# Performance work log

Hardware: AMD Instinct MI355X
Metric: run time of the kernel (lower is better)

The kernel has to match this reference:

```python
import jax, jax.numpy as jnp
import numpy as np

B, T, V, E, U = 1024, 256, 50000, 512, 1024

def setup_inputs() -> dict:
    key = jax.random.key(0)
    ks = jax.random.split(key, 10)
    s = lambda k, shape, fan: jax.random.normal(k, shape, dtype=jnp.float32) * (1.0 / np.sqrt(fan))
    return {
        "inputs": jax.random.randint(ks[0], (B, T), 0, V, dtype=jnp.int32),
        "emb": s(ks[1], (V, E), E),
        "W0": s(ks[2], (E, U), E),
        "U0": s(ks[3], (U, U), U),
        "b0": jnp.zeros((U,), jnp.float32),
        "W1": s(ks[4], (U, U), U),
        "U1": s(ks[5], (U, U), U),
        "b1": jnp.zeros((U,), jnp.float32),
        "Wout": s(ks[6], (U, 1), U),
        "bout": jnp.zeros((1,), jnp.float32),
    }

def reference(inputs, emb, W0, U0, b0, W1, U1, b1, Wout, bout):
    x = emb[inputs]                      # [B, T, E] embedding lookup
    xT = jnp.swapaxes(x, 0, 1)           # [T, B, E] time-major for scan
    h0_init = jnp.zeros((inputs.shape[0], U0.shape[0]), x.dtype)
    h1_init = jnp.zeros((inputs.shape[0], U1.shape[0]), x.dtype)

    def step(carry, xt):
        h0, h1 = carry
        h0 = jnp.tanh(xt @ W0 + h0 @ U0 + b0)   # SimpleRNNCell 0 (dropout inactive, inference)
        h1 = jnp.tanh(h0 @ W1 + h1 @ U1 + b1)   # SimpleRNNCell 1
        return (h0, h1), None

    (h0, h1), _ = jax.lax.scan(step, (h0_init, h1_init), xT)
    return jax.nn.sigmoid(h1 @ Wout + bout)      # [B, 1]
```

## Files before the change

### kernel.cpp

```cpp
#include <hip/hip_runtime.h>
#include <hip/hip_cooperative_groups.h>
#include <math.h>

namespace cg = cooperative_groups;

typedef unsigned short u16;
typedef __bf16 bf16x8 __attribute__((ext_vector_type(8)));
typedef float f32x4 __attribute__((ext_vector_type(4)));
typedef unsigned short u16x8 __attribute__((ext_vector_type(8)));
typedef int i32x4 __attribute__((ext_vector_type(4)));

#define NBLK 256
#define NTHR 512
#define BB 1024
#define TT 256
#define EE 512
#define UU 1024
#define K0 1536
#define K1 2048
#define NK0 48
#define NK1 64
#define KTL0 32
#define KTL1 16
#define HN0 ((size_t)BB * K0)
#define HN1 ((size_t)BB * K1)
#define LDS_BYTES 163840

#define ROSTER_BASE 0
#define FLAG_BASE 32
#define EPOCH_BASE (32 + 2048)
#define BAR_INTS 2560

#define AUX_SC0 1

__device__ i32x4 llvm_amdgcn_raw_buffer_load_i32x4(i32x4 srsrc, int voffset, int soffset,
                                                   int aux) __asm("llvm.amdgcn.raw.buffer.load.v4i32");

__device__ __forceinline__ i32x4 make_srd(const void* p) {
  union { const void* p; int i[2]; } u; u.p = p;
  i32x4 r; r.x = u.i[0]; r.y = u.i[1]; r.z = -1; r.w = 0x00020000;
  return r;
}

__device__ __forceinline__ u16 f2bf(float f) {
  unsigned u = __builtin_bit_cast(unsigned, f);
  u += 0x7fffu + ((u >> 16) & 1u);
  return (u16)(u >> 16);
}
__device__ __forceinline__ float bf2f(u16 h) {
  return __builtin_bit_cast(float, ((unsigned)h) << 16);
}
__device__ __forceinline__ float fast_tanh(float x) {
  x = fminf(fmaxf(x, -15.f), 15.f);
  float e = __expf(2.f * x);
  return (e - 1.f) / (e + 1.f);
}

template<int K, int KLOW>
__device__ __forceinline__ void wfill(u16* __restrict__ Wt,
    const float* __restrict__ Wl, const float* __restrict__ Wh, int gstart) {
  constexpr int NK = K / 32;
  constexpr int NG = 1024 * K / 8;
  for (int g = gstart; g < NG; g += NBLK * NTHR) {
    const int lane = g & 63;
    const int r = g >> 6;
    const int kt = r % NK;
    const int cb = r / NK;
    const int n = cb * 16 + (lane & 15);
    const int kb = kt * 32 + (lane >> 4) * 8;
    u16x8 o;
#pragma unroll
    for (int e = 0; e < 8; ++e) {
      const int k = kb + e;
      const float v = (k < KLOW) ? Wl[(size_t)k * UU + n] : Wh[(size_t)(k - KLOW) * UU + n];
      o[e] = f2bf(v);
    }
    *(u16x8*)(Wt + (size_t)g * 8) = o;
  }
}

__device__ __forceinline__ void xbar(int* __restrict__ bar, int xcc, int slot, int nx,
                                     int tgt, int tid) {
  __syncthreads();
  if (tid < 64) {
    if (tid == 0)
      __hip_atomic_store(&bar[FLAG_BASE + xcc * 256 + slot], tgt,
                         __ATOMIC_RELAXED, __HIP_MEMORY_SCOPE_AGENT);
    if (slot == 0) {
      for (int base = 0; base < nx; base += 64) {
        const int i = base + tid;
        const bool act = (i < nx);
        int guard = 0;
        bool done = false;
        do {
          int v = act ? __hip_atomic_load(&bar[FLAG_BASE + xcc * 256 + i],
                                          __ATOMIC_RELAXED, __HIP_MEMORY_SCOPE_AGENT)
                      : tgt;
          done = __all(v >= tgt) != 0;
        } while (!done && ++guard < 300000);
      }
      if (tid == 0)
        __hip_atomic_store(&bar[EPOCH_BASE + xcc * 32], tgt,
                           __ATOMIC_RELAXED, __HIP_MEMORY_SCOPE_AGENT);
    } else if (tid == 0) {
      int guard = 0;
      while (__hip_atomic_load(&bar[EPOCH_BASE + xcc * 32],
                               __ATOMIC_RELAXED, __HIP_MEMORY_SCOPE_AGENT) < tgt
             && ++guard < 600000)
        __builtin_amdgcn_s_sleep(8);
    }
  }
  __syncthreads();
}

__device__ __forceinline__ void mf1(const i32x4& av,
    const u16* __restrict__ p0, const u16* __restrict__ p1,
    const u16* __restrict__ q2, const u16* __restrict__ q3,
    size_t koff, int lo, f32x4 (&acc)[4]) {
  u16x8 b0 = *(const u16x8*)(p0 + koff + lo);
  u16x8 b1 = *(const u16x8*)(p1 + koff + lo);
  u16x8 b2 = *(const u16x8*)(q2 + koff + lo);
  u16x8 b3 = *(const u16x8*)(q3 + koff + lo);
  bf16x8 fa0 = __builtin_bit_cast(bf16x8, av);
  bf16x8 fb0 = __builtin_bit_cast(bf16x8, b0);
  bf16x8 fb1 = __builtin_bit_cast(bf16x8, b1);
  bf16x8 fb2 = __builtin_bit_cast(bf16x8, b2);
  bf16x8 fb3 = __builtin_bit_cast(bf16x8, b3);
  acc[0] = __builtin_amdgcn_mfma_f32_16x16x32_bf16(fa0, fb0, acc[0], 0, 0, 0);
  acc[1] = __builtin_amdgcn_mfma_f32_16x16x32_bf16(fa0, fb1, acc[1], 0, 0, 0);
  acc[2] = __builtin_amdgcn_mfma_f32_16x16x32_bf16(fa0, fb2, acc[2], 0, 0, 0);
  acc[3] = __builtin_amdgcn_mfma_f32_16x16x32_bf16(fa0, fb3, acc[3], 0, 0, 0);
}

template<int K, int KTL>
__device__ __forceinline__ void gemm2(const i32x4& srdA, int voA,
    const u16* __restrict__ bA, const u16* __restrict__ bB,
    const u16* __restrict__ bP, int lane, f32x4 (&acc)[4]) {
  constexpr int NK = K / 32;
  constexpr int NG = NK / 8;
  const int lo = lane * 8;
  const u16* p0 = bA;
  const u16* p1 = bA + (size_t)NK * 512;
  const u16* bP3 = bP + (size_t)KTL * 512;
  const u16* bB3 = bB + (size_t)NK * 512;

  i32x4 aE[8], aO[8];
#pragma unroll
  for (int j = 0; j < 8; ++j)
    aE[j] = llvm_amdgcn_raw_buffer_load_i32x4(srdA, voA + j * 64, 0, AUX_SC0);

#pragma unroll
  for (int g = 0; g < NG; ++g) {
    if (g + 1 < NG) {
#pragma unroll
      for (int j = 0; j < 8; ++j) {
        if ((g & 1) == 0)
          aO[j] = llvm_amdgcn_raw_buffer_load_i32x4(srdA, voA + ((g + 1) * 8 + j) * 64, 0, AUX_SC0);
        else
          aE[j] = llvm_amdgcn_raw_buffer_load_i32x4(srdA, voA + ((g + 1) * 8 + j) * 64, 0, AUX_SC0);
      }
    }
#pragma unroll
    for (int j = 0; j < 8; ++j) {
      const int kt = g * 8 + j;
      const bool pre = (KTL > 0) && (kt < KTL);
      const u16* q2 = pre ? bP : bB;
      const u16* q3 = pre ? bP3 : bB3;
      if ((g & 1) == 0) mf1(aE[j], p0, p1, q2, q3, (size_t)kt * 512, lo, acc);
      else              mf1(aO[j], p0, p1, q2, q3, (size_t)kt * 512, lo, acc);
    }
  }
}

__device__ __forceinline__ void do_l0(int tk, int xcc, int jl, bool uselds,
    const u16* __restrict__ ldsb, const u16* __restrict__ Wt0,
    const int* __restrict__ inputs, const float* __restrict__ emb,
    const float* __restrict__ b0, u16* __restrict__ A0, u16* __restrict__ A1,
    int tid)
{
  const int lane = tid & 63, w = tid >> 6, q = lane >> 4, l16 = lane & 15;
  const int c0 = jl * 64;
  if (tk < TT - 1) {
    const int grow = xcc * 128 + jl * 8 + (tid >> 6);
    const int c = (tid & 63) * 8;
    const int idx = inputs[grow * TT + tk + 1];
    const f32x4* s = (const f32x4*)(emb + (size_t)idx * EE + c);
    f32x4 f0 = s[0], f1 = s[1];
    u16x8 oa;
#pragma unroll
    for (int j = 0; j < 4; ++j) { oa[j] = f2bf(f0[j]); oa[j + 4] = f2bf(f1[j]); }
    *(u16x8*)(A0 + (size_t)((tk + 1) & 1) * HN0 + (size_t)grow * K0 + c) = oa;
  }
  if (tk < TT) {
    f32x4 acc[4];
#pragma unroll
    for (int n = 0; n < 4; ++n) acc[n] = (f32x4){0.f, 0.f, 0.f, 0.f};
    i32x4 srdA = make_srd(A0 + (size_t)(tk & 1) * HN0);
    const int voA = ((xcc * 128 + w * 16 + l16) * K0 + q * 8) * 2;
    const u16* gA = Wt0 + (size_t)(c0 / 16) * NK0 * 512;
    const u16* bB = Wt0 + (size_t)(c0 / 16 + 2) * NK0 * 512;
    if (uselds) gemm2<K0, KTL0>(srdA, voA, ldsb, bB,
                                ldsb + (size_t)2 * NK0 * 512, lane, acc);
    else        gemm2<K0, 0   >(srdA, voA, gA, bB, ldsb, lane, acc);
    u16* d1 = A1 + (size_t)(tk & 1) * HN1;
    u16* d2 = A0 + (size_t)((tk + 1) & 1) * HN0 + 512;
#pragma unroll
    for (int n = 0; n < 4; ++n) {
      const int col = c0 + n * 16 + l16;
      const float bs = b0[col];
#pragma unroll
      for (int rr = 0; rr < 4; ++rr) {
        const int grow = xcc * 128 + w * 16 + q * 4 + rr;
        const u16 v = f2bf(fast_tanh(acc[n][rr] + bs));
        d1[(size_t)grow * K1 + col] = v;
        d2[(size_t)grow * K0 + col] = v;
      }
    }
  }
}

__device__ __forceinline__ void do_l1(int tk, int xcc, int jl, bool uselds,
    const u16* __restrict__ ldsb, const u16* __restrict__ Wt1,
    const float* __restrict__ b1, u16* __restrict__ A1, int tid)
{
  const int lane = tid & 63, w = tid >> 6, q = lane >> 4, l16 = lane & 15;
  const int c0 = jl * 64;
  f32x4 acc[4];
#pragma unroll
  for (int n = 0; n < 4; ++n) acc[n] = (f32x4){0.f, 0.f, 0.f, 0.f};
  i32x4 srdA = make_srd(A1 + (size_t)((tk - 1) & 1) * HN1);
  const int voA = ((xcc * 128 + w * 16 + l16) * K1 + q * 8) * 2;
  const u16* gA = Wt1 + (size_t)(c0 / 16) * NK1 * 512;
  const u16* bB = Wt1 + (size_t)(c0 / 16 + 2) * NK1 * 512;
  if (uselds) gemm2<K1, KTL1>(srdA, voA, ldsb, bB,
                              ldsb + (size_t)2 * NK1 * 512, lane, acc);
  else        gemm2<K1, 0   >(srdA, voA, gA, bB, ldsb, lane, acc);
  u16* d1 = A1 + (size_t)(tk & 1) * HN1 + 1024;
#pragma unroll
  for (int n = 0; n < 4; ++n) {
    const int col = c0 + n * 16 + l16;
    const float bs = b1[col];
#pragma unroll
    for (int rr = 0; rr < 4; ++rr) {
      const int grow = xcc * 128 + w * 16 + q * 4 + rr;
      d1[(size_t)grow * K1 + col] = f2bf(fast_tanh(acc[n][rr] + bs));
    }
  }
}

__global__ __launch_bounds__(NTHR, 2)
void rnn_kernel(const int* __restrict__ inputs, const float* __restrict__ emb,
    const float* __restrict__ W0, const float* __restrict__ U0, const float* __restrict__ b0,
    const float* __restrict__ W1, const float* __restrict__ U1, const float* __restrict__ b1,
    const float* __restrict__ Wout, const float* __restrict__ bout,
    float* __restrict__ out,
    u16* __restrict__ Wt0, u16* __restrict__ Wt1,
    u16* __restrict__ A0, u16* __restrict__ A1, int* __restrict__ bar)
{
  extern __shared__ u16 lds[];
  int* li = (int*)lds;
  cg::grid_group grid = cg::this_grid();
  const int tid = threadIdx.x, bid = blockIdx.x;

  const int gstart = bid * NTHR + tid;
  wfill<K0, 512>(Wt0, W0, U0, gstart);
  wfill<K1, 1024>(Wt1, W1, U1, gstart);
  for (int g = gstart; g < BB * EE / 8; g += NBLK * NTHR) {
    const int b = g >> 6, seg = g & 63;
    const int idx = inputs[b * TT];
    const f32x4* s = (const f32x4*)(emb + (size_t)idx * EE + seg * 8);
    f32x4 f0 = s[0], f1 = s[1];
    u16x8 o;
#pragma unroll
    for (int j = 0; j < 4; ++j) { o[j] = f2bf(f0[j]); o[j + 4] = f2bf(f1[j]); }
    *(u16x8*)(A0 + (size_t)b * K0 + seg * 8) = o;
  }
  {
    const u16x8 z = {0, 0, 0, 0, 0, 0, 0, 0};
    for (int g = gstart; g < BB * 1024 / 8; g += NBLK * NTHR) {
      const int b = g >> 7, seg = g & 127;
      *(u16x8*)(A0 + (size_t)b * K0 + 512 + seg * 8) = z;
      *(u16x8*)(A1 + (size_t)b * K1 + 1024 + seg * 8) = z;
    }
  }
  if (bid == 0) for (int i = tid; i < BAR_INTS; i += NTHR) bar[i] = 0;
  grid.sync();

  if (tid == 0) {
    const int xc = __builtin_amdgcn_s_getreg((7 << 11) | 20) & 7;
    li[0] = xc;
    li[1] = atomicAdd(&bar[ROSTER_BASE + xc], 1);
  }
  __syncthreads();
  const int xcc = li[0], slot = li[1];
  __syncthreads();
  grid.sync();
  if (tid == 0)
    li[0] = __hip_atomic_load(&bar[ROSTER_BASE + xcc],
                              __ATOMIC_RELAXED, __HIP_MEMORY_SCOPE_AGENT);
  __syncthreads();
  const int nx = li[0];
  __syncthreads();

  if (slot < 32) {
    const bool pL0 = slot < 16;
    const int cb = (pL0 ? slot : slot - 16) * 4;
    const int NKp = pL0 ? NK0 : NK1;
    const int KTLp = pL0 ? KTL0 : KTL1;
    const u16* W = pL0 ? Wt0 : Wt1;
    const u16x8* s = (const u16x8*)(W + (size_t)cb * NKp * 512);
    const int nv = 2 * NKp * 64;
    u16x8* d = (u16x8*)lds;
    for (int i = tid; i < nv; i += NTHR) d[i] = s[i];
    u16x8* d2 = d + nv;
    const int nv2 = 2 * KTLp * 64;
    for (int i = tid; i < nv2; i += NTHR) {
      const int f = i / (KTLp * 64);
      const int rem = i - f * (KTLp * 64);
      d2[i] = *((const u16x8*)(W + (size_t)(cb + 2 + f) * NKp * 512) + rem);
    }
  }
  __syncthreads();

  for (int tk = 0; tk <= TT; ++tk) {
    for (int job = slot; job < 32; job += nx) {
      const bool uselds = (job == slot);
      if (job < 16) do_l0(tk, xcc, job, uselds, lds, Wt0, inputs, emb, b0, A0, A1, tid);
      else if (tk >= 1) do_l1(tk, xcc, job - 16, uselds, lds, Wt1, b1, A1, tid);
    }
    xbar(bar, xcc, slot, nx, tk + 1, tid);
  }

  if (slot == 0) {
    const int lane = tid & 63, w = tid >> 6;
    i32x4 srdH = make_srd(A1);
    const f32x4* wv = (const f32x4*)(Wout + lane * 16);
    f32x4 w0 = wv[0], w1 = wv[1], w2 = wv[2], w3 = wv[3];
    for (int rr = 0; rr < 16; ++rr) {
      const int grow = xcc * 128 + w * 16 + rr;
      const int vo = (grow * K1 + 1024 + lane * 16) * 2;
      i32x4 hv0 = llvm_amdgcn_raw_buffer_load_i32x4(srdH, vo, 0, AUX_SC0);
      i32x4 hv1 = llvm_amdgcn_raw_buffer_load_i32x4(srdH, vo + 16, 0, AUX_SC0);
      u16x8 lo = __builtin_bit_cast(u16x8, hv0);
      u16x8 hi = __builtin_bit_cast(u16x8, hv1);
      float s = 0.f;
#pragma unroll
      for (int j = 0; j < 4; ++j) {
        s += bf2f(lo[j]) * w0[j];
        s += bf2f(lo[j + 4]) * w1[j];
        s += bf2f(hi[j]) * w2[j];
        s += bf2f(hi[j + 4]) * w3[j];
      }
#pragma unroll
      for (int off = 32; off > 0; off >>= 1) s += __shfl_down(s, off);
      if (lane == 0) out[grow] = 1.f / (1.f + expf(-(s + bout[0])));
    }
  }
}

extern "C" void kernel_launch(void* const* d_in, const int* in_sizes, int n_in,
                              void* d_out, int out_size, void* d_ws, size_t ws_size,
                              hipStream_t stream)
{
  (void)in_sizes; (void)n_in; (void)out_size; (void)ws_size;
  const int*   inputs = (const int*)d_in[0];
  const float* emb    = (const float*)d_in[1];
  const float* W0     = (const float*)d_in[2];
  const float* U0     = (const float*)d_in[3];
  const float* b0     = (const float*)d_in[4];
  const float* W1     = (const float*)d_in[5];
  const float* U1     = (const float*)d_in[6];
  const float* b1     = (const float*)d_in[7];
  const float* Wout   = (const float*)d_in[8];
  const float* bout   = (const float*)d_in[9];
  float* out = (float*)d_out;

  u16* Wt0 = (u16*)d_ws;
  u16* Wt1 = Wt0 + (size_t)1024 * K0;
  u16* A0  = Wt1 + (size_t)1024 * K1;
  u16* A1  = A0 + (size_t)2 * 1024 * K0;
  int* bar = (int*)(A1 + (size_t)2 * 1024 * K1);

  static int lds_set = 0;
  if (!lds_set) {
    hipFuncSetAttribute((const void*)rnn_kernel,
                        hipFuncAttributeMaxDynamicSharedMemorySize, LDS_BYTES);
    lds_set = 1;
  }

  void* args[] = { &inputs, &emb, &W0, &U0, &b0, &W1, &U1, &b1, &Wout, &bout,
                   &out, &Wt0, &Wt1, &A0, &A1, &bar };
  hipLaunchCooperativeKernel((void*)rnn_kernel, dim3(NBLK), dim3(NTHR), args, LDS_BYTES, stream);
}
```

Before: 6.482 ms.

## Software-pipeline global B-operand loads in the recurrent GEMM tail and simplify KTL=0 path

Splits gemm2 into an LDS-resident prefix phase and a global-memory suffix phase. In the suffix, the non-LDS B tiles are prefetched one group ahead through buffer loads into double-buffered registers, rather than loaded synchronously in place. The KTL=0 path becomes a simple unrolled loop with no A prefetch. This aims to hide global-memory latency on the streamed weight slice, at the cost of more register pressure and possibly a less-pipelined KTL=0 path.

Result: slower. 6.855 ms (+5.8%).

```diff
diff --git a/kernel.cpp b/kernel.cpp
--- a/kernel.cpp
+++ b/kernel.cpp
@@ -32,6 +32,7 @@
 #define BAR_INTS 2560
 
 #define AUX_SC0 1
+#define AUX_L1  0
 
 __device__ i32x4 llvm_amdgcn_raw_buffer_load_i32x4(i32x4 srsrc, int voffset, int soffset,
                                                    int aux) __asm("llvm.amdgcn.raw.buffer.load.v4i32");
@@ -132,42 +133,98 @@
   acc[3] = __builtin_amdgcn_mfma_f32_16x16x32_bf16(fa0, fb3, acc[3], 0, 0, 0);
 }
 
+__device__ __forceinline__ void mf1r(const i32x4& av,
+    const u16* __restrict__ p0, const u16* __restrict__ p1,
+    size_t koff, int lo, const i32x4& b2v, const i32x4& b3v, f32x4 (&acc)[4]) {
+  u16x8 b0 = *(const u16x8*)(p0 + koff + lo);
+  u16x8 b1 = *(const u16x8*)(p1 + koff + lo);
+  bf16x8 fa0 = __builtin_bit_cast(bf16x8, av);
+  bf16x8 fb0 = __builtin_bit_cast(bf16x8, b0);
+  bf16x8 fb1 = __builtin_bit_cast(bf16x8, b1);
+  bf16x8 fb2 = __builtin_bit_cast(bf16x8, b2v);
+  bf16x8 fb3 = __builtin_bit_cast(bf16x8, b3v);
+  acc[0] = __builtin_amdgcn_mfma_f32_16x16x32_bf16(fa0, fb0, acc[0], 0, 0, 0);
+  acc[1] = __builtin_amdgcn_mfma_f32_16x16x32_bf16(fa0, fb1, acc[1], 0, 0, 0);
+  acc[2] = __builtin_amdgcn_mfma_f32_16x16x32_bf16(fa0, fb2, acc[2], 0, 0, 0);
+  acc[3] = __builtin_amdgcn_mfma_f32_16x16x32_bf16(fa0, fb3, acc[3], 0, 0, 0);
+}
+
 template<int K, int KTL>
 __device__ __forceinline__ void gemm2(const i32x4& srdA, int voA,
     const u16* __restrict__ bA, const u16* __restrict__ bB,
     const u16* __restrict__ bP, int lane, f32x4 (&acc)[4]) {
   constexpr int NK = K / 32;
-  constexpr int NG = NK / 8;
   const int lo = lane * 8;
-  const u16* p0 = bA;
-  const u16* p1 = bA + (size_t)NK * 512;
-  const u16* bP3 = bP + (size_t)KTL * 512;
-  const u16* bB3 = bB + (size_t)NK * 512;
-
-  i32x4 aE[8], aO[8];
-#pragma unroll
-  for (int j = 0; j < 8; ++j)
-    aE[j] = llvm_amdgcn_raw_buffer_load_i32x4(srdA, voA + j * 64, 0, AUX_SC0);
-
-#pragma unroll
-  for (int g = 0; g < NG; ++g) {
-    if (g + 1 < NG) {
+
+  if constexpr (KTL == 0) {
+    const u16* p0 = bA;
+    const u16* p1 = bA + (size_t)NK * 512;
+    const u16* q2 = bB;
+    const u16* q3 = bB + (size_t)NK * 512;
+#pragma unroll 8
+    for (int kt = 0; kt < NK; ++kt) {
+      i32x4 a0 = llvm_amdgcn_raw_buffer_load_i32x4(srdA, voA + kt * 64, 0, AUX_SC0);
+      mf1(a0, p0, p1, q2, q3, (size_t)kt * 512, lo, acc);
+    }
+  } else {
+    constexpr int NGP = KTL / 8;
+    constexpr int NGS = (NK - KTL) / 4;
+    const u16* p0 = bA;
+    const u16* p1 = bA + (size_t)NK * 512;
+    const u16* bP3 = bP + (size_t)KTL * 512;
+    i32x4 srdB = make_srd(bB);
+    const int lob = lane * 16;
+
+    i32x4 aE[8], aO[8];
+    i32x4 sAE[4], sBE[8], sAO[4], sBO[8];
+
+#pragma unroll
+    for (int j = 0; j < 8; ++j)
+      aE[j] = llvm_amdgcn_raw_buffer_load_i32x4(srdA, voA + j * 64, 0, AUX_SC0);
+
+#pragma unroll
+    for (int g = 0; g < NGP; ++g) {
+      if (g + 1 < NGP) {
+#pragma unroll
+        for (int j = 0; j < 8; ++j) {
+          i32x4 v = llvm_amdgcn_raw_buffer_load_i32x4(srdA, voA + ((g + 1) * 8 + j) * 64, 0, AUX_SC0);
+          if ((g & 1) == 0) aO[j] = v; else aE[j] = v;
+        }
+      } else {
+#pragma unroll
+        for (int j = 0; j < 4; ++j) {
+          sAE[j] = llvm_amdgcn_raw_buffer_load_i32x4(srdA, voA + (KTL + j) * 64, 0, AUX_SC0);
+          sBE[2 * j]     = llvm_amdgcn_raw_buffer_load_i32x4(srdB, (0 * NK + KTL + j) * 1024 + lob, 0, AUX_L1);
+          sBE[2 * j + 1] = llvm_amdgcn_raw_buffer_load_i32x4(srdB, (1 * NK + KTL + j) * 1024 + lob, 0, AUX_L1);
+        }
+      }
 #pragma unroll
       for (int j = 0; j < 8; ++j) {
-        if ((g & 1) == 0)
-          aO[j] = llvm_amdgcn_raw_buffer_load_i32x4(srdA, voA + ((g + 1) * 8 + j) * 64, 0, AUX_SC0);
-        else
-          aE[j] = llvm_amdgcn_raw_buffer_load_i32x4(srdA, voA + ((g + 1) * 8 + j) * 64, 0, AUX_SC0);
-      }
-    }
-#pragma unroll
-    for (int j = 0; j < 8; ++j) {
-      const int kt = g * 8 + j;
-      const bool pre = (KTL > 0) && (kt < KTL);
-      const u16* q2 = pre ? bP : bB;
-      const u16* q3 = pre ? bP3 : bB3;
-      if ((g & 1) == 0) mf1(aE[j], p0, p1, q2, q3, (size_t)kt * 512, lo, acc);
-      else              mf1(aO[j], p0, p1, q2, q3, (size_t)kt * 512, lo, acc);
+        const int kt = g * 8 + j;
+        if ((g & 1) == 0) mf1(aE[j], p0, p1, bP, bP3, (size_t)kt * 512, lo, acc);
+        else              mf1(aO[j], p0, p1, bP, bP3, (size_t)kt * 512, lo, acc);
+      }
+    }
+
+#pragma unroll
+    for (int s = 0; s < NGS; ++s) {
+      if (s + 1 < NGS) {
+        const int kb = KTL + (s + 1) * 4;
+#pragma unroll
+        for (int j = 0; j < 4; ++j) {
+          i32x4 va = llvm_amdgcn_raw_buffer_load_i32x4(srdA, voA + (kb + j) * 64, 0, AUX_SC0);
+          i32x4 v2 = llvm_amdgcn_raw_buffer_load_i32x4(srdB, (0 * NK + kb + j) * 1024 + lob, 0, AUX_L1);
+          i32x4 v3 = llvm_amdgcn_raw_buffer_load_i32x4(srdB, (1 * NK + kb + j) * 1024 + lob, 0, AUX_L1);
+          if ((s & 1) == 0) { sAO[j] = va; sBO[2 * j] = v2; sBO[2 * j + 1] = v3; }
+          else              { sAE[j] = va; sBE[2 * j] = v2; sBE[2 * j + 1] = v3; }
+        }
+      }
+#pragma unroll
+      for (int j = 0; j < 4; ++j) {
+        const int kt = KTL + s * 4 + j;
+        if ((s & 1) == 0) mf1r(sAE[j], p0, p1, (size_t)kt * 512, lo, sBE[2 * j], sBE[2 * j + 1], acc);
+        else              mf1r(sAO[j], p0, p1, (size_t)kt * 512, lo, sBO[2 * j], sBO[2 * j + 1], acc);
+      }
     }
   }
 }
```
